# Kernel tuning notes

Hardware: AMD Instinct MI355X
Metric: run time of the kernel (lower is better)

## Reference

```python
import jax, jax.numpy as jnp
import numpy as np

RANK = 4
IN_FEATURES = 1024
OUT_FEATURES = 1024
ALPHA = 1.0
SCALING = ALPHA / RANK


def setup_inputs() -> dict:
    key = jax.random.key(0)
    kx, ka = jax.random.split(key)
    x = jax.random.normal(kx, (4, 8192, IN_FEATURES), dtype=jnp.float32)
    # kaiming_uniform_(a=sqrt(5)) on [rank, in_features]: bound = sqrt(3) * gain / sqrt(fan_in)
    # gain = sqrt(2/(1+a^2)) = sqrt(1/3); fan_in = in_features -> bound = 1/sqrt(in_features)
    bound = 1.0 / np.sqrt(IN_FEATURES)
    lora_A = jax.random.uniform(ka, (RANK, IN_FEATURES), dtype=jnp.float32, minval=-bound, maxval=bound)
    # original init is zeros for B; use random values so the output/gradients are non-trivial
    lora_B = jax.random.normal(jax.random.fold_in(key, 7), (OUT_FEATURES, RANK), dtype=jnp.float32) * 0.02
    return {"x": x, "lora_A": lora_A, "lora_B": lora_B}


def reference(x, lora_A, lora_B):
    # h = scaling * (x @ A^T) @ B^T   (dropout p=0 -> identity)
    h = jnp.einsum('bsi,ri->bsr', x, lora_A)      # [B, S, rank]
    h = jnp.einsum('bsr,or->bso', h, lora_B)      # [B, S, out_features]
    return h * SCALING
```

## Files before the change

### kernel.cpp

```cpp
#include <hip/hip_runtime.h>
#include <stdint.h>

#define IN_F 1024
#define OUT_F 1024
#define SCALING 0.25f
#define TILE_ROWS 16
#define CHUNK_COLS 256
#define NCHUNK (IN_F / CHUNK_COLS)
#define ROW_PITCH 260
#define BLOCK 256

typedef __attribute__((address_space(3))) unsigned int as3_u32;
typedef const __attribute__((address_space(1))) unsigned int as1_u32;

__device__ __forceinline__ void row_to_lds(const float* g, const float* lds_row,
                                           int lane) {
  __builtin_amdgcn_global_load_lds(
      (as1_u32*)(uintptr_t)(g + lane * 4),
      (as3_u32*)(uint32_t)(uintptr_t)(lds_row),
      16, 0, 0);
}

__global__ __launch_bounds__(BLOCK) void lora_tile(
    const float* __restrict__ x, const float* __restrict__ A,
    const float* __restrict__ B, float* __restrict__ out, int nrows) {
  __shared__ float4 As4[4 * 256];
  __shared__ float xs[2][TILE_ROWS * ROW_PITCH];
  __shared__ float4 hf[TILE_ROWS];

  const int t = threadIdx.x;
  const int lane = t & 63;
  const int wave = t >> 6;
  const int row0 = blockIdx.x * TILE_ROWS;
  if (row0 >= nrows) return;

  const float4* __restrict__ B4 = (const float4*)B;
  const float4 bf0 = B4[4 * t + 0];
  const float4 bf1 = B4[4 * t + 1];
  const float4 bf2 = B4[4 * t + 2];
  const float4 bf3 = B4[4 * t + 3];

  const float4* __restrict__ A4 = (const float4*)A;
#pragma unroll
  for (int k = 0; k < 4; ++k) As4[t + 256 * k] = A4[t + 256 * k];
  __syncthreads();

#pragma unroll
  for (int r = 0; r < 4; ++r) {
    const int row = wave * 4 + r;
    row_to_lds(x + (size_t)(row0 + row) * IN_F, &xs[0][row * ROW_PITCH], lane);
  }

  const int lrow = lane >> 4;
  const int seg = lane & 15;
  const int myrow = wave * 4 + lrow;

  float h0 = 0.f, h1 = 0.f, h2 = 0.f, h3 = 0.f;

#pragma unroll
  for (int c = 0; c < NCHUNK; ++c) {
    if (c + 1 < NCHUNK) {
#pragma unroll
      for (int r = 0; r < 4; ++r) {
        const int row = wave * 4 + r;
        row_to_lds(x + (size_t)(row0 + row) * IN_F + (c + 1) * CHUNK_COLS,
                   &xs[(c + 1) & 1][row * ROW_PITCH], lane);
      }
      __builtin_amdgcn_s_waitcnt(0xF74);
    } else {
      __builtin_amdgcn_s_waitcnt(0xF70);
    }
    __asm__ __volatile__("" ::: "memory");

    const float4* __restrict__ xr4 =
        (const float4*)&xs[c & 1][myrow * ROW_PITCH + seg * 16];
#pragma unroll
    for (int j = 0; j < 4; ++j) {
      const float4 xv = xr4[j];
      const int ai = c * 64 + seg * 4 + j;
      const float4 a0 = As4[0 * 256 + ai];
      const float4 a1 = As4[1 * 256 + ai];
      const float4 a2 = As4[2 * 256 + ai];
      const float4 a3 = As4[3 * 256 + ai];
      h0 += xv.x * a0.x + xv.y * a0.y + xv.z * a0.z + xv.w * a0.w;
      h1 += xv.x * a1.x + xv.y * a1.y + xv.z * a1.z + xv.w * a1.w;
      h2 += xv.x * a2.x + xv.y * a2.y + xv.z * a2.z + xv.w * a2.w;
      h3 += xv.x * a3.x + xv.y * a3.y + xv.z * a3.z + xv.w * a3.w;
    }
  }

#pragma unroll
  for (int off = 1; off < 16; off <<= 1) {
    h0 += __shfl_xor(h0, off, 64);
    h1 += __shfl_xor(h1, off, 64);
    h2 += __shfl_xor(h2, off, 64);
    h3 += __shfl_xor(h3, off, 64);
  }
  if (seg == 0)
    hf[myrow] = make_float4(h0 * SCALING, h1 * SCALING, h2 * SCALING,
                            h3 * SCALING);
  __syncthreads();

  float4* __restrict__ out4 = (float4*)out;
#pragma unroll
  for (int r = 0; r < TILE_ROWS; ++r) {
    const float4 h = hf[r];
    float4 res;
    res.x = h.x * bf0.x + h.y * bf0.y + h.z * bf0.z + h.w * bf0.w;
    res.y = h.x * bf1.x + h.y * bf1.y + h.z * bf1.z + h.w * bf1.w;
    res.z = h.x * bf2.x + h.y * bf2.y + h.z * bf2.z + h.w * bf2.w;
    res.w = h.x * bf3.x + h.y * bf3.y + h.z * bf3.z + h.w * bf3.w;
    out4[(size_t)(row0 + r) * (OUT_F / 4) + t] = res;
  }
}

extern "C" void kernel_launch(void* const* d_in, const int* in_sizes, int n_in,
                              void* d_out, int out_size, void* d_ws,
                              size_t ws_size, hipStream_t stream) {
  const float* x = (const float*)d_in[0];
  const float* A = (const float*)d_in[1];
  const float* B = (const float*)d_in[2];
  float* out = (float*)d_out;

  const int nrows = in_sizes[0] / IN_F;
  const int blocks = (nrows + TILE_ROWS - 1) / TILE_ROWS;
  lora_tile<<<blocks, BLOCK, 0, stream>>>(x, A, B, out, nrows);
}
```

Baseline: 235.5 us.

## Stream x rows through registers and keep A in registers, dropping LDS staging

Replaces the global_load_lds double-buffered staging of x and the LDS copy of A with direct register loads. Each wave processes one full row per iteration, prefetching the next row into a second register buffer, and does a full 64-lane shuffle reduction per row. The B loads move after the reduction and launch bounds ask for 3 blocks per CU. This removes LDS traffic and most of the shared memory use, so occupancy can rise, but it raises register pressure and adds more shuffle reductions.

```diff
diff --git a/kernel.cpp b/kernel.cpp
--- a/kernel.cpp
+++ b/kernel.cpp
@@ -5,27 +5,11 @@
 #define OUT_F 1024
 #define SCALING 0.25f
 #define TILE_ROWS 16
-#define CHUNK_COLS 256
-#define NCHUNK (IN_F / CHUNK_COLS)
-#define ROW_PITCH 260
 #define BLOCK 256
 
-typedef __attribute__((address_space(3))) unsigned int as3_u32;
-typedef const __attribute__((address_space(1))) unsigned int as1_u32;
-
-__device__ __forceinline__ void row_to_lds(const float* g, const float* lds_row,
-                                           int lane) {
-  __builtin_amdgcn_global_load_lds(
-      (as1_u32*)(uintptr_t)(g + lane * 4),
-      (as3_u32*)(uint32_t)(uintptr_t)(lds_row),
-      16, 0, 0);
-}
-
-__global__ __launch_bounds__(BLOCK) void lora_tile(
+__global__ __launch_bounds__(BLOCK, 3) void lora_tile(
     const float* __restrict__ x, const float* __restrict__ A,
     const float* __restrict__ B, float* __restrict__ out, int nrows) {
-  __shared__ float4 As4[4 * 256];
-  __shared__ float xs[2][TILE_ROWS * ROW_PITCH];
   __shared__ float4 hf[TILE_ROWS];
 
   const int t = threadIdx.x;
@@ -34,72 +18,58 @@
   const int row0 = blockIdx.x * TILE_ROWS;
   if (row0 >= nrows) return;
 
+  const float4* __restrict__ A4 = (const float4*)A;
+  float4 a[4][4];
+#pragma unroll
+  for (int r = 0; r < 4; ++r)
+#pragma unroll
+    for (int k = 0; k < 4; ++k) a[r][k] = A4[r * 256 + lane + 64 * k];
+
+  const float4* __restrict__ x4 =
+      (const float4*)(x + (size_t)(row0 + wave * 4) * IN_F);
+
+  float4 xr[2][4];
+#pragma unroll
+  for (int k = 0; k < 4; ++k) xr[0][k] = x4[lane + 64 * k];
+
+#pragma unroll
+  for (int i = 0; i < 4; ++i) {
+    if (i + 1 < 4) {
+#pragma unroll
+      for (int k = 0; k < 4; ++k)
+        xr[(i + 1) & 1][k] = x4[(i + 1) * 256 + lane + 64 * k];
+    }
+    float p0 = 0.f, p1 = 0.f, p2 = 0.f, p3 = 0.f;
+#pragma unroll
+    for (int k = 0; k < 4; ++k) {
+      const float4 xv = xr[i & 1][k];
+      p0 += xv.x * a[0][k].x + xv.y * a[0][k].y + xv.z * a[0][k].z +
+            xv.w * a[0][k].w;
+      p1 += xv.x * a[1][k].x + xv.y * a[1][k].y + xv.z * a[1][k].z +
+            xv.w * a[1][k].w;
+      p2 += xv.x * a[2][k].x + xv.y * a[2][k].y + xv.z * a[2][k].z +
+            xv.w * a[2][k].w;
+      p3 += xv.x * a[3][k].x + xv.y * a[3][k].y + xv.z * a[3][k].z +
+            xv.w * a[3][k].w;
+    }
+#pragma unroll
+    for (int off = 1; off < 64; off <<= 1) {
+      p0 += __shfl_xor(p0, off, 64);
+      p1 += __shfl_xor(p1, off, 64);
+      p2 += __shfl_xor(p2, off, 64);
+      p3 += __shfl_xor(p3, off, 64);
+    }
+    if (lane == 0)
+      hf[wave * 4 + i] = make_float4(p0 * SCALING, p1 * SCALING, p2 * SCALING,
+                                     p3 * SCALING);
+  }
+  __syncthreads();
+
   const float4* __restrict__ B4 = (const float4*)B;
   const float4 bf0 = B4[4 * t + 0];
   const float4 bf1 = B4[4 * t + 1];
   const float4 bf2 = B4[4 * t + 2];
   const float4 bf3 = B4[4 * t + 3];
-
-  const float4* __restrict__ A4 = (const float4*)A;
-#pragma unroll
-  for (int k = 0; k < 4; ++k) As4[t + 256 * k] = A4[t + 256 * k];
-  __syncthreads();
-
-#pragma unroll
-  for (int r = 0; r < 4; ++r) {
-    const int row = wave * 4 + r;
-    row_to_lds(x + (size_t)(row0 + row) * IN_F, &xs[0][row * ROW_PITCH], lane);
-  }
-
-  const int lrow = lane >> 4;
-  const int seg = lane & 15;
-  const int myrow = wave * 4 + lrow;
-
-  float h0 = 0.f, h1 = 0.f, h2 = 0.f, h3 = 0.f;
-
-#pragma unroll
-  for (int c = 0; c < NCHUNK; ++c) {
-    if (c + 1 < NCHUNK) {
-#pragma unroll
-      for (int r = 0; r < 4; ++r) {
-        const int row = wave * 4 + r;
-        row_to_lds(x + (size_t)(row0 + row) * IN_F + (c + 1) * CHUNK_COLS,
-                   &xs[(c + 1) & 1][row * ROW_PITCH], lane);
-      }
-      __builtin_amdgcn_s_waitcnt(0xF74);
-    } else {
-      __builtin_amdgcn_s_waitcnt(0xF70);
-    }
-    __asm__ __volatile__("" ::: "memory");
-
-    const float4* __restrict__ xr4 =
-        (const float4*)&xs[c & 1][myrow * ROW_PITCH + seg * 16];
-#pragma unroll
-    for (int j = 0; j < 4; ++j) {
-      const float4 xv = xr4[j];
-      const int ai = c * 64 + seg * 4 + j;
-      const float4 a0 = As4[0 * 256 + ai];
-      const float4 a1 = As4[1 * 256 + ai];
-      const float4 a2 = As4[2 * 256 + ai];
-      const float4 a3 = As4[3 * 256 + ai];
-      h0 += xv.x * a0.x + xv.y * a0.y + xv.z * a0.z + xv.w * a0.w;
-      h1 += xv.x * a1.x + xv.y * a1.y + xv.z * a1.z + xv.w * a1.w;
-      h2 += xv.x * a2.x + xv.y * a2.y + xv.z * a2.z + xv.w * a2.w;
-      h3 += xv.x * a3.x + xv.y * a3.y + xv.z * a3.z + xv.w * a3.w;
-    }
-  }
-
-#pragma unroll
-  for (int off = 1; off < 16; off <<= 1) {
-    h0 += __shfl_xor(h0, off, 64);
-    h1 += __shfl_xor(h1, off, 64);
-    h2 += __shfl_xor(h2, off, 64);
-    h3 += __shfl_xor(h3, off, 64);
-  }
-  if (seg == 0)
-    hf[myrow] = make_float4(h0 * SCALING, h1 * SCALING, h2 * SCALING,
-                            h3 * SCALING);
-  __syncthreads();
 
   float4* __restrict__ out4 = (float4*)out;
 #pragma unroll
```

After: 232.5 us. No clear change (-1.3%).
